# Kernel tuning notes

Hardware: AMD Instinct MI355X
Metric: run time of the kernel (lower is better)

The kernel has to match this reference:

```python
import jax, jax.numpy as jnp
import numpy as np

DIM = 512          # model dim
K = 4              # max_block_size (depthwise conv kernel size)
DS = 4             # downsample_factor
BLOCKS = (1, 2, 3, 4)  # block sizes, all offset 0
MULT = 12          # lcm(1,2,3,4) = block_pad_multiple
VOCAB = 256


def setup_inputs() -> dict:
    key = jax.random.key(0)
    ks = jax.random.split(key, 7)
    x = jax.random.randint(ks[0], (4, 4096), 0, VOCAB)
    emb = jax.random.normal(ks[1], (VOCAB, DIM), dtype=jnp.float32) * 0.02
    dw_w = jax.random.normal(ks[2], (DIM, 1, K), dtype=jnp.float32) * 0.1   # depthwise conv weight [out, in/groups, k]
    dw_b = jnp.zeros((DIM,), dtype=jnp.float32)
    pw_w = jax.random.normal(ks[3], (DIM, DIM), dtype=jnp.float32) * 0.05   # 1x1 conv weight [out, in]
    pw_b = jnp.zeros((DIM,), dtype=jnp.float32)
    score_w = jax.random.normal(ks[4], (DIM,), dtype=jnp.float32) * 0.05    # Linear(dim,1)
    score_b = jnp.zeros((), dtype=jnp.float32)
    return {"x": x, "emb": emb, "dw_w": dw_w, "dw_b": dw_b,
            "pw_w": pw_w, "pw_b": pw_b, "score_w": score_w, "score_b": score_b}


def _gbst(x, emb, dw_w, dw_b, pw_w, pw_b, score_w, score_b):
    b, n = x.shape
    m = ((n + DS - 1) // DS) * DS  # next multiple of downsample factor
    xe = emb[x]  # [b, n, d]

    # positional: Pad seq end by K-1, depthwise conv1d(k=K), then 1x1 conv
    xp = jnp.pad(xe, ((0, 0), (0, K - 1), (0, 0)))
    xc = jnp.transpose(xp, (0, 2, 1))  # [b, d, n+K-1]
    y = jax.lax.conv_general_dilated(
        xc, dw_w, window_strides=(1,), padding='VALID',
        dimension_numbers=('NCH', 'OIH', 'NCH'), feature_group_count=DIM)
    y = y + dw_b[None, :, None]                       # [b, d, n]
    y = jnp.einsum('ed,bdn->bne', pw_w, y) + pw_b     # [b, n, d]

    # pad seq to multiple of lcm of block sizes
    L = ((n + MULT - 1) // MULT) * MULT
    xpad = jnp.pad(y, ((0, 0), (0, L - n), (0, 0)))   # [b, L, d]

    # multi-scale block mean pooling, broadcast back to full length
    reprs = []
    for bs in BLOCKS:
        br = xpad.reshape(b, L // bs, bs, DIM).mean(axis=2)  # [b, L/bs, d]
        reprs.append(jnp.repeat(br, bs, axis=1))             # [b, L, d]
    block_reprs = jnp.stack(reprs, axis=2)  # [b, L, nblocks, d]

    # learned block scoring + softmax over block sizes
    scores = jnp.einsum('blkd,d->blk', block_reprs, score_w) + score_b
    scores = jax.nn.softmax(scores, axis=2)  # [b, L, nblocks]

    # consensus attention over positions (inner dim = nblocks)
    sim = jnp.einsum('bik,bjk->bij', scores, scores)  # [b, L, L]
    attn = jax.nn.softmax(sim, axis=-1)
    scores = jnp.einsum('bij,bjk->bik', attn, scores)

    out = jnp.einsum('blkd,blk->bld', block_reprs, scores)  # [b, L, d]
    out = out[:, :m]
    out = out.reshape(b, m // DS, DS, DIM).mean(axis=2)     # [b, m/DS, d]
    return out


def reference(x, emb, dw_w, dw_b, pw_w, pw_b, score_w, score_b):
    return _gbst(x, emb, dw_w, dw_b, pw_w, pw_b, score_w, score_b)
```

## Files before the change

### kernel.cpp

```cpp
#include <hip/hip_runtime.h>
#include <hip/hip_bf16.h>

#define DIMD 512
#define NSEQ 4096
#define LPAD 4104
#define NCH 12
#define CH 342
#define SPLITS 8
#define PT_BK 32

#define OFF_P      0u
#define OFF_CONST  524288u
#define OFF_Q      524800u
#define OFF_AACC   525824u
#define OFF_PPART  591488u

__global__ __launch_bounds__(256) void k_ptable(
    const float* __restrict__ emb, const float* __restrict__ dw_w,
    const float* __restrict__ pw_w, float* __restrict__ Ppart) {
  __shared__ float As[PT_BK][68];
  __shared__ float Bs[PT_BK][68];
  const int tid = threadIdx.x;
  const int m0 = blockIdx.x * 64;
  const int e0 = blockIdx.y * 64;
  const int z  = blockIdx.z;
  const int kk = m0 >> 8;
  const int v0 = m0 & 255;
  const int srow = tid >> 3;
  const int sd4  = (tid & 7) * 4;
  const int ty = tid >> 4, tx = tid & 15;
  float c[4][4] = {};
  for (int kt = 0; kt < 64; kt += PT_BK) {
    const int d0 = z * 64 + kt;
    const float dw0 = dw_w[(d0 + sd4 + 0) * 4 + kk];
    const float dw1 = dw_w[(d0 + sd4 + 1) * 4 + kk];
    const float dw2 = dw_w[(d0 + sd4 + 2) * 4 + kk];
    const float dw3 = dw_w[(d0 + sd4 + 3) * 4 + kk];
    #pragma unroll
    for (int rr = 0; rr < 2; ++rr) {
      const int row = srow + rr * 32;
      float4 ev = *reinterpret_cast<const float4*>(&emb[(v0 + row) * DIMD + d0 + sd4]);
      As[sd4 + 0][row] = ev.x * dw0;
      As[sd4 + 1][row] = ev.y * dw1;
      As[sd4 + 2][row] = ev.z * dw2;
      As[sd4 + 3][row] = ev.w * dw3;
      float4 bv = *reinterpret_cast<const float4*>(&pw_w[(e0 + row) * DIMD + d0 + sd4]);
      Bs[sd4 + 0][row] = bv.x;
      Bs[sd4 + 1][row] = bv.y;
      Bs[sd4 + 2][row] = bv.z;
      Bs[sd4 + 3][row] = bv.w;
    }
    __syncthreads();
    #pragma unroll
    for (int q = 0; q < PT_BK; ++q) {
      float4 a = *reinterpret_cast<const float4*>(&As[q][ty * 4]);
      float4 b = *reinterpret_cast<const float4*>(&Bs[q][tx * 4]);
      c[0][0] += a.x * b.x; c[0][1] += a.x * b.y; c[0][2] += a.x * b.z; c[0][3] += a.x * b.w;
      c[1][0] += a.y * b.x; c[1][1] += a.y * b.y; c[1][2] += a.y * b.z; c[1][3] += a.y * b.w;
      c[2][0] += a.z * b.x; c[2][1] += a.z * b.y; c[2][2] += a.z * b.z; c[2][3] += a.z * b.w;
      c[3][0] += a.w * b.x; c[3][1] += a.w * b.y; c[3][2] += a.w * b.z; c[3][3] += a.w * b.w;
    }
    __syncthreads();
  }
  #pragma unroll
  for (int i = 0; i < 4; ++i) {
    *reinterpret_cast<float4*>(
        &Ppart[(size_t)z * 524288u + (m0 + ty * 4 + i) * DIMD + e0 + tx * 4]) =
        make_float4(c[i][0], c[i][1], c[i][2], c[i][3]);
  }
}

__global__ __launch_bounds__(256) void k_pcomb(
    const float* __restrict__ Ppart, float* __restrict__ P,
    const float* __restrict__ pw_w, const float* __restrict__ pw_b,
    const float* __restrict__ dw_b, const float* __restrict__ score_w,
    float* __restrict__ constv, float* __restrict__ q) {
  __shared__ float qred[4];
  const int tid = threadIdx.x;
  const int idx = blockIdx.x * 256 + tid;
  const float4* p4 = reinterpret_cast<const float4*>(Ppart);
  float4 a = p4[idx];
  #pragma unroll
  for (int zz = 1; zz < SPLITS; ++zz) {
    float4 v = p4[(size_t)zz * 131072u + idx];
    a.x += v.x; a.y += v.y; a.z += v.z; a.w += v.w;
  }
  reinterpret_cast<float4*>(P)[idx] = a;
  float4 sw = reinterpret_cast<const float4*>(score_w)[idx & 127];
  float part = a.x * sw.x + a.y * sw.y + a.z * sw.z + a.w * sw.w;
  for (int off = 32; off > 0; off >>= 1) part += __shfl_down(part, off);
  if ((tid & 63) == 0) qred[tid >> 6] = part;
  __syncthreads();
  if (tid == 0)   q[blockIdx.x * 2 + 0] = qred[0] + qred[1];
  if (tid == 128) q[blockIdx.x * 2 + 1] = qred[2] + qred[3];
  if (blockIdx.x < 2) {
    const int e = blockIdx.x * 256 + tid;
    float acc = pw_b[e];
    const float4* pr = reinterpret_cast<const float4*>(&pw_w[e * DIMD]);
    const float4* db = reinterpret_cast<const float4*>(dw_b);
    for (int d4 = 0; d4 < DIMD / 4; ++d4) {
      float4 w = pr[d4]; float4 bb = db[d4];
      acc += w.x * bb.x + w.y * bb.y + w.z * bb.z + w.w * bb.w;
    }
    constv[e] = acc;
  }
}

__global__ __launch_bounds__(256) void k_attn(
    const int* __restrict__ x, const float* __restrict__ q,
    const float* __restrict__ constv, const float* __restrict__ score_w,
    const float* __restrict__ score_b_p, float* __restrict__ Aacc) {
  __shared__ float qlds[1024];
  __shared__ float tli[264];
  __shared__ float tlj[348];
  __shared__ float4 sch[CH];
  __shared__ float c0red[2];
  const int b = blockIdx.z;
  const int c = blockIdx.y;
  const int i0 = blockIdx.x * 256;
  const int j0 = c * CH;
  const int tid = threadIdx.x;
  reinterpret_cast<float4*>(qlds)[tid] = reinterpret_cast<const float4*>(q)[tid];
  if (tid < 128) {
    float4 cv = reinterpret_cast<const float4*>(constv)[tid];
    float4 sw = reinterpret_cast<const float4*>(score_w)[tid];
    float part = cv.x * sw.x + cv.y * sw.y + cv.z * sw.z + cv.w * sw.w;
    for (int off = 32; off > 0; off >>= 1) part += __shfl_down(part, off);
    if ((tid & 63) == 0) c0red[tid >> 6] = part;
  }
  __syncthreads();
  const float c0 = c0red[0] + c0red[1];
  const int* xb = &x[b * NSEQ];
  auto tval = [&](int l) -> float {
    if ((unsigned)l >= (unsigned)NSEQ) return 0.f;
    float acc = c0;
    #pragma unroll
    for (int k = 0; k < 4; ++k) {
      const int pos = l + k;
      if (pos < NSEQ) acc += qlds[(k << 8) + xb[pos]];
    }
    return acc;
  };
  for (int idx = tid; idx < 261; idx += 256) tli[idx] = tval(i0 - 2 + idx);
  for (int idx = tid; idx < 347; idx += 256) tlj[idx] = tval(j0 - 2 + idx);
  __syncthreads();
  const float sb = score_b_p[0];
  for (int idx = tid; idx < CH; idx += 256) {
    const int l = j0 + idx;
    #define TJ(j) tlj[(j) - j0 + 2]
    float p0 = TJ(l) + sb;
    int j2 = l & ~1;
    float p1 = (TJ(j2) + TJ(j2 + 1)) * 0.5f + sb;
    int j3 = (l / 3) * 3;
    float p2 = (TJ(j3) + TJ(j3 + 1) + TJ(j3 + 2)) * (1.0f / 3.0f) + sb;
    int j4 = l & ~3;
    float p3 = (TJ(j4) + TJ(j4 + 1) + TJ(j4 + 2) + TJ(j4 + 3)) * 0.25f + sb;
    #undef TJ
    float mx = fmaxf(fmaxf(p0, p1), fmaxf(p2, p3));
    float e0 = __expf(p0 - mx), e1 = __expf(p1 - mx);
    float e2 = __expf(p2 - mx), e3 = __expf(p3 - mx);
    float inv = 1.0f / (e0 + e1 + e2 + e3);
    sch[idx] = make_float4(e0 * inv, e1 * inv, e2 * inv, e3 * inv);
  }
  const int i = i0 + tid;
  float4 si;
  {
    const int l = i;
    #define TI(j) tli[(j) - i0 + 2]
    float p0 = TI(l) + sb;
    int j2 = l & ~1;
    float p1 = (TI(j2) + TI(j2 + 1)) * 0.5f + sb;
    int j3 = (l / 3) * 3;
    float p2 = (TI(j3) + TI(j3 + 1) + TI(j3 + 2)) * (1.0f / 3.0f) + sb;
    int j4 = l & ~3;
    float p3 = (TI(j4) + TI(j4 + 1) + TI(j4 + 2) + TI(j4 + 3)) * 0.25f + sb;
    #undef TI
    float mx = fmaxf(fmaxf(p0, p1), fmaxf(p2, p3));
    float e0 = __expf(p0 - mx), e1 = __expf(p1 - mx);
    float e2 = __expf(p2 - mx), e3 = __expf(p3 - mx);
    float inv = 1.0f / (e0 + e1 + e2 + e3);
    si = make_float4(e0 * inv, e1 * inv, e2 * inv, e3 * inv);
  }
  __syncthreads();
  if (i >= LPAD) return;
  float a0x = 0.f, a0y = 0.f, a0z = 0.f, a0w = 0.f;
  float a1x = 0.f, a1y = 0.f, a1z = 0.f, a1w = 0.f;
  #pragma unroll 3
  for (int jj = 0; jj < CH; jj += 2) {
    float4 u = sch[jj];
    float4 v = sch[jj + 1];
    float d0 = si.x * u.x + si.y * u.y + si.z * u.z + si.w * u.w;
    float d1 = si.x * v.x + si.y * v.y + si.z * v.z + si.w * v.w;
    float e0 = __expf(d0), e1 = __expf(d1);
    a0x += e0 * u.x; a0y += e0 * u.y; a0z += e0 * u.z; a0w += e0 * u.w;
    a1x += e1 * v.x; a1y += e1 * v.y; a1z += e1 * v.z; a1w += e1 * v.w;
  }
  float* aa = &Aacc[((size_t)(b * LPAD) + i) * 4];
  atomicAdd(aa + 0, a0x + a1x);
  atomicAdd(aa + 1, a0y + a1y);
  atomicAdd(aa + 2, a0z + a1z);
  atomicAdd(aa + 3, a0w + a1w);
}

__global__ __launch_bounds__(128) void k_out(
    const int* __restrict__ x, const float* __restrict__ P,
    const float* __restrict__ constv, const float* __restrict__ Aacc,
    float* __restrict__ out) {
  const int b = blockIdx.y;
  const int g0 = blockIdx.x * 4;
  const int tl = threadIdx.x;
  const int R0 = 4 * g0 - 2;
  __shared__ float coef[4][20];
  if (tl < 80) (&coef[0][0])[tl] = 0.f;
  __syncthreads();
  if (tl < 4) {
    const int g = g0 + tl;
    const float4* a4 = reinterpret_cast<const float4*>(Aacc) + (size_t)b * LPAD;
    for (int dl = 0; dl < 4; ++dl) {
      const int l = 4 * g + dl;
      float4 av = a4[l];
      float inv = 1.0f / (av.x + av.y + av.z + av.w);
      float sk[4] = {av.x * inv, av.y * inv, av.z * inv, av.w * inv};
      for (int k = 0; k < 4; ++k) {
        const int bs = k + 1;
        const int j0 = (l / bs) * bs;
        const float wv = sk[k] / (float)(bs * 4);
        for (int jj = 0; jj < bs; ++jj) coef[tl][j0 + jj - R0] += wv;
      }
    }
  }
  __syncthreads();
  const int* xb = &x[b * NSEQ];
  const float4 cv = reinterpret_cast<const float4*>(constv)[tl];
  float4 acc0 = {0.f, 0.f, 0.f, 0.f}, acc1 = {0.f, 0.f, 0.f, 0.f};
  float4 acc2 = {0.f, 0.f, 0.f, 0.f}, acc3 = {0.f, 0.f, 0.f, 0.f};
  for (int r = 0; r < 20; ++r) {
    const int row = R0 + r;
    if ((unsigned)row >= (unsigned)NSEQ) continue;
    const float c0 = coef[0][r], c1 = coef[1][r];
    const float c2 = coef[2][r], c3 = coef[3][r];
    if (c0 + c1 + c2 + c3 == 0.f) continue;
    float yx = cv.x, yy = cv.y, yz = cv.z, yw = cv.w;
    #pragma unroll
    for (int k = 0; k < 4; ++k) {
      const int pos = row + k;
      if (pos < NSEQ) {
        const int tok = xb[pos];
        const float4 pv = *reinterpret_cast<const float4*>(
            &P[((unsigned)(k << 8) + tok) * DIMD + tl * 4]);
        yx += pv.x; yy += pv.y; yz += pv.z; yw += pv.w;
      }
    }
    acc0.x += c0 * yx; acc0.y += c0 * yy; acc0.z += c0 * yz; acc0.w += c0 * yw;
    acc1.x += c1 * yx; acc1.y += c1 * yy; acc1.z += c1 * yz; acc1.w += c1 * yw;
    acc2.x += c2 * yx; acc2.y += c2 * yy; acc2.z += c2 * yz; acc2.w += c2 * yw;
    acc3.x += c3 * yx; acc3.y += c3 * yy; acc3.z += c3 * yz; acc3.w += c3 * yw;
  }
  float4* o = reinterpret_cast<float4*>(out) + ((size_t)(b * 1024) + g0) * 128 + tl;
  o[0 * 128] = acc0;
  o[1 * 128] = acc1;
  o[2 * 128] = acc2;
  o[3 * 128] = acc3;
}

extern "C" void kernel_launch(void* const* d_in, const int* in_sizes, int n_in,
                              void* d_out, int out_size, void* d_ws, size_t ws_size,
                              hipStream_t stream) {
  const int* x = (const int*)d_in[0];
  const float* emb = (const float*)d_in[1];
  const float* dw_w = (const float*)d_in[2];
  const float* dw_b = (const float*)d_in[3];
  const float* pw_w = (const float*)d_in[4];
  const float* pw_b = (const float*)d_in[5];
  const float* score_w = (const float*)d_in[6];
  const float* score_b = (const float*)d_in[7];
  float* out = (float*)d_out;
  float* ws = (float*)d_ws;
  float* P      = ws + OFF_P;
  float* constv = ws + OFF_CONST;
  float* q      = ws + OFF_Q;
  float* Aacc   = ws + OFF_AACC;
  float* Ppart  = ws + OFF_PPART;

  hipMemsetAsync(Aacc, 0, (size_t)4 * LPAD * 4 * sizeof(float), stream);
  k_ptable<<<dim3(16, 8, SPLITS), 256, 0, stream>>>(emb, dw_w, pw_w, Ppart);
  k_pcomb<<<512, 256, 0, stream>>>(Ppart, P, pw_w, pw_b, dw_b, score_w, constv, q);
  k_attn<<<dim3(17, NCH, 4), 256, 0, stream>>>(x, q, constv, score_w, score_b, Aacc);
  k_out<<<dim3(256, 4), 128, 0, stream>>>(x, P, constv, Aacc, out);
}
```

Before: 149.3 us.

## Fuse split-K reduction into ptable via last-block counter; use exp2 in attention

Removes the separate k_pcomb launch. The last split-K block for each output tile, found with an atomic counter and threadfence, now reduces the partials, writes P, atomically accumulates q and computes constv. The workspace is reordered so that a single memset zeroes Aacc, q and the counters. The attention inner loop pre-scales the scores by log2(e) and uses the hardware exp2 builtin, saving a multiply per exponential. In exchange, q now depends on float atomics, so summation order is nondeterministic, and the larger memset adds a little work.

After: 252.8 us. +69.4%, slower.

```diff
diff --git a/kernel.cpp b/kernel.cpp
--- a/kernel.cpp
+++ b/kernel.cpp
@@ -9,17 +9,23 @@
 #define SPLITS 8
 #define PT_BK 32
 
-#define OFF_P      0u
-#define OFF_CONST  524288u
-#define OFF_Q      524800u
-#define OFF_AACC   525824u
-#define OFF_PPART  591488u
+#define OFF_AACC   0u
+#define OFF_Q      65664u
+#define OFF_CNT    66688u
+#define OFF_CONST  66816u
+#define OFF_P      67328u
+#define OFF_PPART  591616u
 
 __global__ __launch_bounds__(256) void k_ptable(
     const float* __restrict__ emb, const float* __restrict__ dw_w,
-    const float* __restrict__ pw_w, float* __restrict__ Ppart) {
+    const float* __restrict__ pw_w, const float* __restrict__ pw_b,
+    const float* __restrict__ dw_b, const float* __restrict__ score_w,
+    float* __restrict__ Ppart, float* __restrict__ P,
+    float* __restrict__ q, int* __restrict__ cnt,
+    float* __restrict__ constv) {
   __shared__ float As[PT_BK][68];
   __shared__ float Bs[PT_BK][68];
+  __shared__ int lastFlag;
   const int tid = threadIdx.x;
   const int m0 = blockIdx.x * 64;
   const int e0 = blockIdx.y * 64;
@@ -52,9 +58,9 @@
     }
     __syncthreads();
     #pragma unroll
-    for (int q = 0; q < PT_BK; ++q) {
-      float4 a = *reinterpret_cast<const float4*>(&As[q][ty * 4]);
-      float4 b = *reinterpret_cast<const float4*>(&Bs[q][tx * 4]);
+    for (int qq = 0; qq < PT_BK; ++qq) {
+      float4 a = *reinterpret_cast<const float4*>(&As[qq][ty * 4]);
+      float4 b = *reinterpret_cast<const float4*>(&Bs[qq][tx * 4]);
       c[0][0] += a.x * b.x; c[0][1] += a.x * b.y; c[0][2] += a.x * b.z; c[0][3] += a.x * b.w;
       c[1][0] += a.y * b.x; c[1][1] += a.y * b.y; c[1][2] += a.y * b.z; c[1][3] += a.y * b.w;
       c[2][0] += a.z * b.x; c[2][1] += a.z * b.y; c[2][2] += a.z * b.z; c[2][3] += a.z * b.w;
@@ -68,41 +74,50 @@
         &Ppart[(size_t)z * 524288u + (m0 + ty * 4 + i) * DIMD + e0 + tx * 4]) =
         make_float4(c[i][0], c[i][1], c[i][2], c[i][3]);
   }
-}
-
-__global__ __launch_bounds__(256) void k_pcomb(
-    const float* __restrict__ Ppart, float* __restrict__ P,
-    const float* __restrict__ pw_w, const float* __restrict__ pw_b,
-    const float* __restrict__ dw_b, const float* __restrict__ score_w,
-    float* __restrict__ constv, float* __restrict__ q) {
-  __shared__ float qred[4];
-  const int tid = threadIdx.x;
-  const int idx = blockIdx.x * 256 + tid;
-  const float4* p4 = reinterpret_cast<const float4*>(Ppart);
-  float4 a = p4[idx];
+  __threadfence();
+  if (tid == 0) {
+    int old = atomicAdd(&cnt[blockIdx.y * 16 + blockIdx.x], 1);
+    lastFlag = (old == SPLITS - 1) ? 1 : 0;
+  }
+  __syncthreads();
+  if (!lastFlag) return;
+  __threadfence();
+  const float4* pp4 = reinterpret_cast<const float4*>(Ppart);
+  float4* p4 = reinterpret_cast<float4*>(P);
+  const float4* sw4 = reinterpret_cast<const float4*>(score_w);
+  const int row = tid >> 2;
+  const int c4  = (tid & 3) * 4;
+  float qpart = 0.f;
   #pragma unroll
-  for (int zz = 1; zz < SPLITS; ++zz) {
-    float4 v = p4[(size_t)zz * 131072u + idx];
-    a.x += v.x; a.y += v.y; a.z += v.z; a.w += v.w;
-  }
-  reinterpret_cast<float4*>(P)[idx] = a;
-  float4 sw = reinterpret_cast<const float4*>(score_w)[idx & 127];
-  float part = a.x * sw.x + a.y * sw.y + a.z * sw.z + a.w * sw.w;
-  for (int off = 32; off > 0; off >>= 1) part += __shfl_down(part, off);
-  if ((tid & 63) == 0) qred[tid >> 6] = part;
-  __syncthreads();
-  if (tid == 0)   q[blockIdx.x * 2 + 0] = qred[0] + qred[1];
-  if (tid == 128) q[blockIdx.x * 2 + 1] = qred[2] + qred[3];
-  if (blockIdx.x < 2) {
-    const int e = blockIdx.x * 256 + tid;
-    float acc = pw_b[e];
-    const float4* pr = reinterpret_cast<const float4*>(&pw_w[e * DIMD]);
-    const float4* db = reinterpret_cast<const float4*>(dw_b);
-    for (int d4 = 0; d4 < DIMD / 4; ++d4) {
+  for (int j = 0; j < 4; ++j) {
+    const int f4 = (m0 + row) * 128 + (e0 >> 2) + c4 + j;
+    float4 a = pp4[f4];
+    #pragma unroll
+    for (int zz = 1; zz < SPLITS; ++zz) {
+      float4 v = pp4[(size_t)zz * 131072u + f4];
+      a.x += v.x; a.y += v.y; a.z += v.z; a.w += v.w;
+    }
+    p4[f4] = a;
+    float4 sv = sw4[(e0 >> 2) + c4 + j];
+    qpart += a.x * sv.x + a.y * sv.y + a.z * sv.z + a.w * sv.w;
+  }
+  qpart += __shfl_xor(qpart, 1);
+  qpart += __shfl_xor(qpart, 2);
+  if ((tid & 3) == 0) atomicAdd(&q[m0 + row], qpart);
+  if (blockIdx.x == 0) {
+    const int e = e0 + (tid >> 2);
+    const int dc = (tid & 3) * 128;
+    float acc = 0.f;
+    const float4* pr = reinterpret_cast<const float4*>(&pw_w[e * DIMD + dc]);
+    const float4* db = reinterpret_cast<const float4*>(&dw_b[dc]);
+    #pragma unroll 8
+    for (int d4 = 0; d4 < 32; ++d4) {
       float4 w = pr[d4]; float4 bb = db[d4];
       acc += w.x * bb.x + w.y * bb.y + w.z * bb.z + w.w * bb.w;
     }
-    constv[e] = acc;
+    acc += __shfl_xor(acc, 1);
+    acc += __shfl_xor(acc, 2);
+    if ((tid & 3) == 0) constv[e] = pw_b[e] + acc;
   }
 }
 
@@ -183,15 +198,19 @@
   }
   __syncthreads();
   if (i >= LPAD) return;
+  const float LOG2E = 1.4426950408889634f;
+  const float s2x = si.x * LOG2E, s2y = si.y * LOG2E;
+  const float s2z = si.z * LOG2E, s2w = si.w * LOG2E;
   float a0x = 0.f, a0y = 0.f, a0z = 0.f, a0w = 0.f;
   float a1x = 0.f, a1y = 0.f, a1z = 0.f, a1w = 0.f;
   #pragma unroll 3
   for (int jj = 0; jj < CH; jj += 2) {
     float4 u = sch[jj];
     float4 v = sch[jj + 1];
-    float d0 = si.x * u.x + si.y * u.y + si.z * u.z + si.w * u.w;
-    float d1 = si.x * v.x + si.y * v.y + si.z * v.z + si.w * v.w;
-    float e0 = __expf(d0), e1 = __expf(d1);
+    float d0 = s2x * u.x + s2y * u.y + s2z * u.z + s2w * u.w;
+    float d1 = s2x * v.x + s2y * v.y + s2z * v.z + s2w * v.w;
+    float e0 = __builtin_amdgcn_exp2f(d0);
+    float e1 = __builtin_amdgcn_exp2f(d1);
     a0x += e0 * u.x; a0y += e0 * u.y; a0z += e0 * u.z; a0w += e0 * u.w;
     a1x += e1 * v.x; a1y += e1 * v.y; a1z += e1 * v.z; a1w += e1 * v.w;
   }
@@ -276,15 +295,16 @@
   const float* score_b = (const float*)d_in[7];
   float* out = (float*)d_out;
   float* ws = (float*)d_ws;
+  float* Aacc   = ws + OFF_AACC;
+  float* q      = ws + OFF_Q;
+  int*   cnt    = (int*)(ws + OFF_CNT);
+  float* constv = ws + OFF_CONST;
   float* P      = ws + OFF_P;
-  float* constv = ws + OFF_CONST;
-  float* q      = ws + OFF_Q;
-  float* Aacc   = ws + OFF_AACC;
   float* Ppart  = ws + OFF_PPART;
 
-  hipMemsetAsync(Aacc, 0, (size_t)4 * LPAD * 4 * sizeof(float), stream);
-  k_ptable<<<dim3(16, 8, SPLITS), 256, 0, stream>>>(emb, dw_w, pw_w, Ppart);
-  k_pcomb<<<512, 256, 0, stream>>>(Ppart, P, pw_w, pw_b, dw_b, score_w, constv, q);
+  hipMemsetAsync(ws, 0, (size_t)66816 * sizeof(float), stream);
+  k_ptable<<<dim3(16, 8, SPLITS), 256, 0, stream>>>(
+      emb, dw_w, pw_w, pw_b, dw_b, score_w, Ppart, P, q, cnt, constv);
   k_attn<<<dim3(17, NCH, 4), 256, 0, stream>>>(x, q, constv, score_w, score_b, Aacc);
   k_out<<<dim3(256, 4), 128, 0, stream>>>(x, P, constv, Aacc, out);
 }
```
